# Kernel tuning notes

Hardware: AMD Instinct MI355X
Metric: run time of the kernel (lower is better)

Reference implementation:

```python
import jax, jax.numpy as jnp
import numpy as np

B, S, D = 16, 1024, 384
H, DH = 6, 64  # head_dim = hidden // heads


def setup_inputs() -> dict:
    key = jax.random.key(0)
    ks = jax.random.split(key, 9)
    std = 0.02
    return {
        "x": jax.random.normal(ks[0], (B, S, D), jnp.float32),
        "Wq": jax.random.normal(ks[1], (H, D, DH), jnp.float32) * std,
        "bq": jax.random.normal(ks[2], (H, DH), jnp.float32) * std,
        "Wk": jax.random.normal(ks[3], (H, D, DH), jnp.float32) * std,
        "bk": jax.random.normal(ks[4], (H, DH), jnp.float32) * std,
        "Wv": jax.random.normal(ks[5], (H, D, DH), jnp.float32) * std,
        "bv": jax.random.normal(ks[6], (H, DH), jnp.float32) * std,
        "Wo": jax.random.normal(ks[7], (D, D), jnp.float32) * std,  # [out, in] like nn.Linear
        "bo": jax.random.normal(ks[8], (D,), jnp.float32) * std,
    }


def reference(x, Wq, bq, Wk, bk, Wv, bv, Wo, bo):
    # Per-head q/k/v projections (stacked over heads h)
    q = jnp.einsum("bsd,hde->bhse", x, Wq) + bq[None, :, None, :]
    k = jnp.einsum("bsd,hde->bhse", x, Wk) + bk[None, :, None, :]
    v = jnp.einsum("bsd,hde->bhse", x, Wv) + bv[None, :, None, :]
    # Explicit softmax attention (dropout prob = 0.0 in config)
    scores = jnp.einsum("bhse,bhte->bhst", q, k) / jnp.sqrt(jnp.float32(DH))
    probs = jax.nn.softmax(scores, axis=-1)
    ctx = jnp.einsum("bhst,bhte->bhse", probs, v)  # [B,H,S,DH]
    # Concat heads along last dim: [B,S,H*DH]
    concat = jnp.transpose(ctx, (0, 2, 1, 3)).reshape(B, S, H * DH)
    # Output projection (nn.Linear: y = x @ W^T + b)
    out = jnp.einsum("bsd,ed->bse", concat, Wo) + bo
    return out
```

## Files before the change

kernel.cpp:

```cpp
#include <hip/hip_runtime.h>
#include <hip/hip_bf16.h>

typedef __attribute__((ext_vector_type(8))) short short8;
typedef __attribute__((ext_vector_type(4))) short short4v;
typedef __attribute__((ext_vector_type(4))) float float4v;
typedef __attribute__((ext_vector_type(4))) int int4v;

#define MFMA16(a,b,c) __builtin_amdgcn_mfma_f32_16x16x32_bf16((a),(b),(c),0,0,0)
#define EXP2(x) __builtin_amdgcn_exp2f(x)

static constexpr int Bz = 16, Sq = 1024, Dm = 384, Hh = 6, Dh = 64;
static constexpr int Mtok = Bz * Sq;
static constexpr int NQKV = 1152;

__device__ __forceinline__ short f2bf(float f) {
  union { float f; unsigned u; } v; v.f = f;
  unsigned r = v.u + 0x7fffu + ((v.u >> 16) & 1u);
  return (short)(r >> 16);
}

__device__ __forceinline__ unsigned cvtpk(float a, float b) {
  unsigned d;
  asm("v_cvt_pk_bf16_f32 %0, %1, %2" : "=v"(d) : "v"(a), "v"(b));
  return d;
}

__device__ __forceinline__ void gload16(const void* src, void* lds) {
  __builtin_amdgcn_global_load_lds(
      (const __attribute__((address_space(1))) unsigned int*)src,
      (__attribute__((address_space(3))) unsigned int*)lds, 16, 0, 0);
}

__device__ __forceinline__ int vperm(int s) {
  return (s & ~31) | ((s & 12) << 1) | ((s & 16) >> 2) | (s & 3);
}

__global__ __launch_bounds__(256) void conv_x(const float* __restrict__ x,
                                              short* __restrict__ xb) {
  const int i = (blockIdx.x * 256 + threadIdx.x) * 8;
  float4v v0 = *(const float4v*)(x + i);
  float4v v1 = *(const float4v*)(x + i + 4);
  short8 o;
  o[0] = f2bf(v0[0]); o[1] = f2bf(v0[1]); o[2] = f2bf(v0[2]); o[3] = f2bf(v0[3]);
  o[4] = f2bf(v1[0]); o[5] = f2bf(v1[1]); o[6] = f2bf(v1[2]); o[7] = f2bf(v1[3]);
  *(short8*)(xb + i) = o;
}

__global__ __launch_bounds__(256) void conv_w(const float* __restrict__ Wq,
                                              const float* __restrict__ Wk,
                                              const float* __restrict__ Wv,
                                              const float* __restrict__ bq,
                                              const float* __restrict__ bk,
                                              const float* __restrict__ bv,
                                              const float* __restrict__ Wo,
                                              short* __restrict__ Wt,
                                              float* __restrict__ bias,
                                              short* __restrict__ Wob) {
  const float SCL = 0.125f * 1.44269504088896340736f;
  const int i = blockIdx.x * 256 + threadIdx.x;
  const int NW = NQKV * Dm;
  if (i < NW) {
    const int c = i / Dm, d = i % Dm;
    const int p = c / 384, rr = c % 384;
    const int h = rr >> 6, dh = rr & 63;
    const float* W = (p == 0) ? Wq : ((p == 1) ? Wk : Wv);
    float w = W[(h * Dm + d) * Dh + dh];
    if (p == 0) w *= SCL;
    Wt[c * Dm + d] = f2bf(w);
  } else if (i < NW + NQKV) {
    const int c = i - NW;
    const int p = c / 384, rr = c % 384;
    const int h = rr >> 6, dh = rr & 63;
    const float* bb = (p == 0) ? bq : ((p == 1) ? bk : bv);
    float b = bb[h * Dh + dh];
    if (p == 0) b *= SCL;
    bias[c] = b;
  } else if (i < NW + NQKV + Dm * Dm) {
    const int j = i - NW - NQKV;
    Wob[j] = f2bf(Wo[j]);
  }
}


__global__ __launch_bounds__(256) void qkv_gemm(const short* __restrict__ Xb,
                                                const short* __restrict__ Wt,
                                                const float* __restrict__ bias,
                                                short* __restrict__ qkv,
                                                short* __restrict__ vt) {
  __shared__ char smem[49152];
  const int tid = threadIdx.x;
  const int wave = tid >> 6, lane = tid & 63;
  const int r = lane & 15, g = lane >> 4;
  const int wr = wave >> 1, wc = wave & 1;

  const int flat = blockIdx.x;
  const int w = (flat & 7) * 144 + (flat >> 3);
  const int bx = w % 9, by = w / 9;
  const int bm0 = by * 128, bn0 = bx * 128;
  const int m0 = bm0 + wr * 64, n0 = bn0 + wc * 64;

  float bv_n[4];
#pragma unroll
  for (int ni = 0; ni < 4; ++ni) bv_n[ni] = bias[n0 + ni * 16 + r];
  asm volatile("s_waitcnt vmcnt(0)" ::: "memory");

  const char *aSrc0, *aSrc1, *bSrc0, *bSrc1;
  {
    const int o0 = tid * 16, o1 = 4096 + tid * 16;
    const int lr0 = o0 >> 7, cb0 = (o0 & 127) ^ ((lr0 & 7) << 4);
    const int lr1 = o1 >> 7, cb1 = (o1 & 127) ^ ((lr1 & 7) << 4);
    const int m_0 = 2 * lr0 + (cb0 >> 6), kb0 = cb0 & 63;
    const int m_1 = 2 * lr1 + (cb1 >> 6), kb1 = cb1 & 63;
    aSrc0 = (const char*)(Xb + (bm0 + m_0) * Dm) + kb0;
    aSrc1 = (const char*)(Xb + (bm0 + m_1) * Dm) + kb1;
    bSrc0 = (const char*)(Wt + (bn0 + m_0) * Dm) + kb0;
    bSrc1 = (const char*)(Wt + (bn0 + m_1) * Dm) + kb1;
  }
  auto stage = [&](int t, int buf) {
    char* base = smem + buf * 16384;
    const int kb = t * 64;
    gload16(aSrc0 + kb, base + wave * 1024);
    gload16(aSrc1 + kb, base + 4096 + wave * 1024);
    gload16(bSrc0 + kb, base + 8192 + wave * 1024);
    gload16(bSrc1 + kb, base + 12288 + wave * 1024);
  };

  int aOff[4], bOff[4];
#pragma unroll
  for (int i = 0; i < 4; ++i) {
    const int m = wr * 64 + i * 16 + r;
    const int lr = m >> 1;
    aOff[i] = lr * 128 + ((((m & 1) << 6) | (16 * g)) ^ ((lr & 7) << 4));
    const int n = wc * 64 + i * 16 + r;
    const int lrn = n >> 1;
    bOff[i] = 8192 + lrn * 128 + ((((n & 1) << 6) | (16 * g)) ^ ((lrn & 7) << 4));
  }

  float4v acc[4][4] = {};
  auto compute = [&](int buf) {
    const char* sb = smem + buf * 16384;
    short8 a[4], b[4];
#pragma unroll
    for (int i = 0; i < 4; ++i) a[i] = *(const short8*)(sb + aOff[i]);
#pragma unroll
    for (int i = 0; i < 4; ++i) b[i] = *(const short8*)(sb + bOff[i]);
#pragma unroll
    for (int mi = 0; mi < 4; ++mi)
#pragma unroll
      for (int ni = 0; ni < 4; ++ni)
        acc[mi][ni] = MFMA16(a[mi], b[ni], acc[mi][ni]);
  };

  stage(0, 0);
  stage(1, 1);
  stage(2, 2);
#pragma unroll 1
  for (int t = 0; t < 10; ++t) {
    asm volatile("s_waitcnt vmcnt(8)" ::: "memory");
    __builtin_amdgcn_s_barrier();
    compute(t % 3);
    __builtin_amdgcn_s_barrier();
    if (t < 9) stage(t + 3, t % 3);
  }
  asm volatile("s_waitcnt vmcnt(4)" ::: "memory");
  __builtin_amdgcn_s_barrier();
  compute(1);
  asm volatile("s_waitcnt vmcnt(0)" ::: "memory");
  __builtin_amdgcn_s_barrier();
  compute(2);

#pragma unroll
  for (int ni = 0; ni < 4; ++ni) {
    const int col = n0 + ni * 16 + r;
    const int p = col / 384, rr2 = col % 384;
    const int h = rr2 >> 6, dh = rr2 & 63;
    const float bv = bv_n[ni];
#pragma unroll
    for (int mi = 0; mi < 4; ++mi) {
#pragma unroll
      for (int rp = 0; rp < 2; ++rp) {
        const unsigned u = cvtpk(acc[mi][ni][2 * rp] + bv,
                                 acc[mi][ni][2 * rp + 1] + bv);
        const short lo = (short)u, hi = (short)(u >> 16);
        const int mg = m0 + mi * 16 + 4 * g + 2 * rp;
        if (p < 2) {
          qkv[mg * NQKV + col] = lo;
          qkv[(mg + 1) * NQKV + col] = hi;
        } else {
          const int bb = mg >> 10, s = mg & 1023;
          const int sp = vperm(s);
          short* vp = vt + ((bb * Hh + h) * Dh + dh) * Sq;
          vp[sp] = lo;
          vp[sp + 1] = hi;
        }
      }
    }
  }
}

__global__ __launch_bounds__(256) void attn(const short* __restrict__ qkv,
                                            const short* __restrict__ vt,
                                            short* __restrict__ ctx) {
  __shared__ char smem[32768];
  const int tid = threadIdx.x;
  const int wave = tid >> 6, lane = tid & 63;
  const int r = lane & 15, g = lane >> 4;
  const int xr = (r & 7) << 4;
  const int flat = blockIdx.x;
  const int w = (flat & 7) * 96 + (flat >> 3);
  const int qb = w & 7, bh = w >> 3;
  const int b = bh / Hh, h = bh % Hh;
  const int tok0 = b * Sq;
  const int qw = qb * 128 + wave * 32;

  short8 qf[2][2];
#pragma unroll
  for (int f = 0; f < 2; ++f) {
    const short* qp = qkv + (tok0 + qw + 16 * f + r) * NQKV + h * Dh;
    qf[f][0] = *(const short8*)(qp + 8 * g);
    qf[f][1] = *(const short8*)(qp + 32 + 8 * g);
  }
  asm volatile("s_waitcnt vmcnt(0)" ::: "memory");

  const short* kg = qkv + tok0 * NQKV + 384 + h * Dh;
  const short* vg = vt + (b * Hh + h) * Dh * Sq;

  const int o0 = wave * 2048 + lane * 16;
  const int row0 = o0 >> 7, cb0 = (o0 & 127) ^ ((row0 & 7) << 4);
  const int o1 = o0 + 1024;
  const int row1 = o1 >> 7, cb1 = (o1 & 127) ^ ((row1 & 7) << 4);

#define STAGE(T, BUFSEL)                                                        \
  {                                                                             \
    char* kb_ = smem + (BUFSEL) * 16384;                                        \
    const int kv_ = (T) * 64;                                                   \
    gload16((const char*)(kg + (kv_ + row0) * NQKV) + cb0, kb_ + wave * 2048);  \
    gload16((const char*)(vg + row0 * Sq + kv_) + cb0, kb_ + 8192 + wave * 2048);\
    gload16((const char*)(kg + (kv_ + row1) * NQKV) + cb1, kb_ + wave * 2048 + 1024);\
    gload16((const char*)(vg + row1 * Sq + kv_) + cb1, kb_ + 8192 + wave * 2048 + 1024);\
  }

  int kOff[4][2], vOff[4][2];
#pragma unroll
  for (int kt = 0; kt < 4; ++kt)
#pragma unroll
    for (int c = 0; c < 2; ++c)
      kOff[kt][c] = (16 * kt + r) * 128 + ((64 * c + 16 * g) ^ xr);
#pragma unroll
  for (int d = 0; d < 4; ++d)
#pragma unroll
    for (int h2 = 0; h2 < 2; ++h2)
      vOff[d][h2] = (16 * d + r) * 128 + ((64 * h2 + 16 * g) ^ xr);

  float4v acc[4][2] = {};
  float lsum[2] = {0.f, 0.f};

  auto compute = [&](int bufsel) {
    const char* kb = smem + bufsel * 16384;
    const char* vb = kb + 8192;
    short8 kf[4][2];
#pragma unroll
    for (int kt = 0; kt < 4; ++kt) {
      kf[kt][0] = *(const short8*)(kb + kOff[kt][0]);
      kf[kt][1] = *(const short8*)(kb + kOff[kt][1]);
    }
    short8 vf[4][2];
#pragma unroll
    for (int d = 0; d < 4; ++d)
#pragma unroll
      for (int h2 = 0; h2 < 2; ++h2)
        vf[d][h2] = *(const short8*)(vb + vOff[d][h2]);
    float4v s[4][2];
    __builtin_amdgcn_s_setprio(1);
#pragma unroll
    for (int kt = 0; kt < 4; ++kt)
#pragma unroll
      for (int f = 0; f < 2; ++f) {
        float4v z = {};
        z = MFMA16(kf[kt][0], qf[f][0], z);
        z = MFMA16(kf[kt][1], qf[f][1], z);
        s[kt][f] = z;
      }
    __builtin_amdgcn_s_setprio(0);
    short8 pa[2][2];
#pragma unroll
    for (int f = 0; f < 2; ++f) {
      float ps = 0.f;
#pragma unroll
      for (int h2 = 0; h2 < 2; ++h2) {
        float e0[4], e1[4];
#pragma unroll
        for (int j = 0; j < 4; ++j) {
          e0[j] = EXP2(s[2 * h2][f][j]);
          e1[j] = EXP2(s[2 * h2 + 1][f][j]);
          ps += e0[j] + e1[j];
        }
        int4v wv;
        wv[0] = (int)cvtpk(e0[0], e0[1]);
        wv[1] = (int)cvtpk(e0[2], e0[3]);
        wv[2] = (int)cvtpk(e1[0], e1[1]);
        wv[3] = (int)cvtpk(e1[2], e1[3]);
        pa[f][h2] = __builtin_bit_cast(short8, wv);
      }
      lsum[f] += ps;
    }
    __builtin_amdgcn_s_setprio(1);
#pragma unroll
    for (int d = 0; d < 4; ++d)
#pragma unroll
      for (int f = 0; f < 2; ++f) {
        acc[d][f] = MFMA16(pa[f][0], vf[d][0], acc[d][f]);
        acc[d][f] = MFMA16(pa[f][1], vf[d][1], acc[d][f]);
      }
    __builtin_amdgcn_s_setprio(0);
  };

  STAGE(0, 0)
  STAGE(1, 1)
#pragma unroll 1
  for (int t = 0; t < 15; ++t) {
    asm volatile("s_waitcnt vmcnt(4)" ::: "memory");
    __builtin_amdgcn_s_barrier();
    compute(t & 1);
    __builtin_amdgcn_s_barrier();
    if (t < 14) STAGE(t + 2, t & 1)
  }
  asm volatile("s_waitcnt vmcnt(0)" ::: "memory");
  __builtin_amdgcn_s_barrier();
  compute(1);

#pragma unroll
  for (int f = 0; f < 2; ++f) {
    lsum[f] += __shfl_xor(lsum[f], 16);
    lsum[f] += __shfl_xor(lsum[f], 32);
  }
#pragma unroll
  for (int f = 0; f < 2; ++f) {
    float il[4];
#pragma unroll
    for (int reg = 0; reg < 4; ++reg) il[reg] = 1.f / __shfl(lsum[f], 4 * g + reg);
#pragma unroll
    for (int d = 0; d < 4; ++d) {
      short* cp = ctx + (tok0 + qw + 16 * f + 4 * g) * Dm + h * Dh + 16 * d + r;
#pragma unroll
      for (int reg = 0; reg < 4; ++reg)
        cp[reg * Dm] = f2bf(acc[d][f][reg] * il[reg]);
    }
  }
}

__global__ __launch_bounds__(256) void out_gemm(const short* __restrict__ ctx,
                                                const short* __restrict__ Wob,
                                                const float* __restrict__ bo,
                                                float* __restrict__ out) {
  __shared__ char smem[49152];
  const int tid = threadIdx.x;
  const int wave = tid >> 6, lane = tid & 63;
  const int r = lane & 15, g = lane >> 4;
  const int wr = wave >> 1, wc = wave & 1;

  const int flat = blockIdx.x;
  const int w = (flat & 7) * 48 + (flat >> 3);
  const int bx = w % 3, by = w / 3;
  const int bm0 = by * 128, bn0 = bx * 128;
  const int m0 = bm0 + wr * 64, n0 = bn0 + wc * 64;

  float bv_n[4];
#pragma unroll
  for (int ni = 0; ni < 4; ++ni) bv_n[ni] = bo[n0 + ni * 16 + r];
  asm volatile("s_waitcnt vmcnt(0)" ::: "memory");

  const char *aSrc0, *aSrc1, *bSrc0, *bSrc1;
  {
    const int o0 = tid * 16, o1 = 4096 + tid * 16;
    const int lr0 = o0 >> 7, cb0 = (o0 & 127) ^ ((lr0 & 7) << 4);
    const int lr1 = o1 >> 7, cb1 = (o1 & 127) ^ ((lr1 & 7) << 4);
    const int m_0 = 2 * lr0 + (cb0 >> 6), kb0 = cb0 & 63;
    const int m_1 = 2 * lr1 + (cb1 >> 6), kb1 = cb1 & 63;
    aSrc0 = (const char*)(ctx + (bm0 + m_0) * Dm) + kb0;
    aSrc1 = (const char*)(ctx + (bm0 + m_1) * Dm) + kb1;
    bSrc0 = (const char*)(Wob + (bn0 + m_0) * Dm) + kb0;
    bSrc1 = (const char*)(Wob + (bn0 + m_1) * Dm) + kb1;
  }
  auto stage = [&](int t, int buf) {
    char* base = smem + buf * 16384;
    const int kb = t * 64;
    gload16(aSrc0 + kb, base + wave * 1024);
    gload16(aSrc1 + kb, base + 4096 + wave * 1024);
    gload16(bSrc0 + kb, base + 8192 + wave * 1024);
    gload16(bSrc1 + kb, base + 12288 + wave * 1024);
  };

  int aOff[4], bOff[4];
#pragma unroll
  for (int i = 0; i < 4; ++i) {
    const int m = wr * 64 + i * 16 + r;
    const int lr = m >> 1;
    aOff[i] = lr * 128 + ((((m & 1) << 6) | (16 * g)) ^ ((lr & 7) << 4));
    const int n = wc * 64 + i * 16 + r;
    const int lrn = n >> 1;
    bOff[i] = 8192 + lrn * 128 + ((((n & 1) << 6) | (16 * g)) ^ ((lrn & 7) << 4));
  }

  float4v acc[4][4] = {};
  auto compute = [&](int buf) {
    const char* sb = smem + buf * 16384;
    short8 a[4], b[4];
#pragma unroll
    for (int i = 0; i < 4; ++i) a[i] = *(const short8*)(sb + aOff[i]);
#pragma unroll
    for (int i = 0; i < 4; ++i) b[i] = *(const short8*)(sb + bOff[i]);
#pragma unroll
    for (int mi = 0; mi < 4; ++mi)
#pragma unroll
      for (int ni = 0; ni < 4; ++ni)
        acc[mi][ni] = MFMA16(a[mi], b[ni], acc[mi][ni]);
  };

  stage(0, 0);
  stage(1, 1);
  stage(2, 2);
#pragma unroll 1
  for (int t = 0; t < 10; ++t) {
    asm volatile("s_waitcnt vmcnt(8)" ::: "memory");
    __builtin_amdgcn_s_barrier();
    compute(t % 3);
    __builtin_amdgcn_s_barrier();
    if (t < 9) stage(t + 3, t % 3);
  }
  asm volatile("s_waitcnt vmcnt(4)" ::: "memory");
  __builtin_amdgcn_s_barrier();
  compute(1);
  asm volatile("s_waitcnt vmcnt(0)" ::: "memory");
  __builtin_amdgcn_s_barrier();
  compute(2);

#pragma unroll
  for (int ni = 0; ni < 4; ++ni) {
    const int col = n0 + ni * 16 + r;
    const float bv = bv_n[ni];
#pragma unroll
    for (int mi = 0; mi < 4; ++mi) {
#pragma unroll
      for (int reg = 0; reg < 4; ++reg) {
        const int mg = m0 + mi * 16 + 4 * g + reg;
        out[mg * Dm + col] = acc[mi][ni][reg] + bv;
      }
    }
  }
}

extern "C" void kernel_launch(void* const* d_in, const int* in_sizes, int n_in,
                              void* d_out, int out_size, void* d_ws, size_t ws_size,
                              hipStream_t stream) {
  const float* x  = (const float*)d_in[0];
  const float* Wq = (const float*)d_in[1];
  const float* bq = (const float*)d_in[2];
  const float* Wk = (const float*)d_in[3];
  const float* bk = (const float*)d_in[4];
  const float* Wv = (const float*)d_in[5];
  const float* bv = (const float*)d_in[6];
  const float* Wo = (const float*)d_in[7];
  const float* bo = (const float*)d_in[8];
  float* out = (float*)d_out;

  char* ws = (char*)d_ws;
  short* Xb   = (short*)(ws);
  short* Wt   = (short*)(ws + 12582912);
  float* bias = (float*)(ws + 13467648);
  short* Wob  = (short*)(ws + 13472256);
  short* qkv  = (short*)(ws + 13767168);
  short* vt   = (short*)(ws + 51515904);
  short* ctx  = (short*)(ws + 64098816);

  conv_x<<<Mtok * Dm / (256 * 8), 256, 0, stream>>>(x, Xb);
  conv_w<<<(NQKV * Dm + NQKV + Dm * Dm + 255) / 256, 256, 0, stream>>>(
      Wq, Wk, Wv, bq, bk, bv, Wo, Wt, bias, Wob);
  qkv_gemm<<<1152, 256, 0, stream>>>(Xb, Wt, bias, qkv, vt);
  attn<<<768, 256, 0, stream>>>(qkv, vt, ctx);
  out_gemm<<<384, 256, 0, stream>>>(ctx, Wob, bo, out);
}
```

Before: 100.4 us.

## Use 3-buffer single-barrier pipelines and compute softmax row sums via MFMA

All three kernels move from a pattern of two barriers per iteration to triple buffering. Each iteration issues the load two tiles ahead into the third buffer, so only one barrier per iteration is needed. The attention kernel grows its LDS to 48KB to hold three K/V stages. It also replaces the scalar exp-sum accumulation and the cross-lane shuffle reduction with extra MFMAs against a vector of bf16 ones, which yields the row sums directly in the accumulator layout. This removes VALU adds and the shuffles but adds MFMA work, and the row sums are now taken from bf16-rounded probabilities.

```diff
diff --git a/kernel.cpp b/kernel.cpp
--- a/kernel.cpp
+++ b/kernel.cpp
@@ -153,14 +153,12 @@
 
   stage(0, 0);
   stage(1, 1);
-  stage(2, 2);
 #pragma unroll 1
   for (int t = 0; t < 10; ++t) {
-    asm volatile("s_waitcnt vmcnt(8)" ::: "memory");
+    asm volatile("s_waitcnt vmcnt(4)" ::: "memory");
     __builtin_amdgcn_s_barrier();
     compute(t % 3);
-    __builtin_amdgcn_s_barrier();
-    if (t < 9) stage(t + 3, t % 3);
+    stage(t + 2, (t + 2) % 3);
   }
   asm volatile("s_waitcnt vmcnt(4)" ::: "memory");
   __builtin_amdgcn_s_barrier();
@@ -201,7 +199,7 @@
 __global__ __launch_bounds__(256) void attn(const short* __restrict__ qkv,
                                             const short* __restrict__ vt,
                                             short* __restrict__ ctx) {
-  __shared__ char smem[32768];
+  __shared__ char smem[49152];
   const int tid = threadIdx.x;
   const int wave = tid >> 6, lane = tid & 63;
   const int r = lane & 15, g = lane >> 4;
@@ -252,8 +250,12 @@
     for (int h2 = 0; h2 < 2; ++h2)
       vOff[d][h2] = (16 * d + r) * 128 + ((64 * h2 + 16 * g) ^ xr);
 
+  short8 ones;
+#pragma unroll
+  for (int j = 0; j < 8; ++j) ones[j] = (short)0x3F80;
+
   float4v acc[4][2] = {};
-  float lsum[2] = {0.f, 0.f};
+  float4v lacc[2] = {};
 
   auto compute = [&](int bufsel) {
     const char* kb = smem + bufsel * 16384;
@@ -284,26 +286,16 @@
     __builtin_amdgcn_s_setprio(0);
     short8 pa[2][2];
 #pragma unroll
-    for (int f = 0; f < 2; ++f) {
-      float ps = 0.f;
+    for (int f = 0; f < 2; ++f)
 #pragma unroll
       for (int h2 = 0; h2 < 2; ++h2) {
-        float e0[4], e1[4];
-#pragma unroll
-        for (int j = 0; j < 4; ++j) {
-          e0[j] = EXP2(s[2 * h2][f][j]);
-          e1[j] = EXP2(s[2 * h2 + 1][f][j]);
-          ps += e0[j] + e1[j];
-        }
         int4v wv;
-        wv[0] = (int)cvtpk(e0[0], e0[1]);
-        wv[1] = (int)cvtpk(e0[2], e0[3]);
-        wv[2] = (int)cvtpk(e1[0], e1[1]);
-        wv[3] = (int)cvtpk(e1[2], e1[3]);
+        wv[0] = (int)cvtpk(EXP2(s[2 * h2][f][0]), EXP2(s[2 * h2][f][1]));
+        wv[1] = (int)cvtpk(EXP2(s[2 * h2][f][2]), EXP2(s[2 * h2][f][3]));
+        wv[2] = (int)cvtpk(EXP2(s[2 * h2 + 1][f][0]), EXP2(s[2 * h2 + 1][f][1]));
+        wv[3] = (int)cvtpk(EXP2(s[2 * h2 + 1][f][2]), EXP2(s[2 * h2 + 1][f][3]));
         pa[f][h2] = __builtin_bit_cast(short8, wv);
       }
-      lsum[f] += ps;
-    }
     __builtin_amdgcn_s_setprio(1);
 #pragma unroll
     for (int d = 0; d < 4; ++d)
@@ -312,33 +304,35 @@
         acc[d][f] = MFMA16(pa[f][0], vf[d][0], acc[d][f]);
         acc[d][f] = MFMA16(pa[f][1], vf[d][1], acc[d][f]);
       }
+#pragma unroll
+    for (int f = 0; f < 2; ++f) {
+      lacc[f] = MFMA16(pa[f][0], ones, lacc[f]);
+      lacc[f] = MFMA16(pa[f][1], ones, lacc[f]);
+    }
     __builtin_amdgcn_s_setprio(0);
   };
 
   STAGE(0, 0)
   STAGE(1, 1)
 #pragma unroll 1
-  for (int t = 0; t < 15; ++t) {
+  for (int t = 0; t < 14; ++t) {
     asm volatile("s_waitcnt vmcnt(4)" ::: "memory");
     __builtin_amdgcn_s_barrier();
-    compute(t & 1);
-    __builtin_amdgcn_s_barrier();
-    if (t < 14) STAGE(t + 2, t & 1)
-  }
-  asm volatile("s_waitcnt vmcnt(0)" ::: "memory");
-  __builtin_amdgcn_s_barrier();
-  compute(1);
-
-#pragma unroll
-  for (int f = 0; f < 2; ++f) {
-    lsum[f] += __shfl_xor(lsum[f], 16);
-    lsum[f] += __shfl_xor(lsum[f], 32);
-  }
+    compute(t % 3);
+    STAGE(t + 2, (t + 2) % 3)
+  }
+  asm volatile("s_waitcnt vmcnt(4)" ::: "memory");
+  __builtin_amdgcn_s_barrier();
+  compute(2);
+  asm volatile("s_waitcnt vmcnt(0)" ::: "memory");
+  __builtin_amdgcn_s_barrier();
+  compute(0);
+
 #pragma unroll
   for (int f = 0; f < 2; ++f) {
     float il[4];
 #pragma unroll
-    for (int reg = 0; reg < 4; ++reg) il[reg] = 1.f / __shfl(lsum[f], 4 * g + reg);
+    for (int reg = 0; reg < 4; ++reg) il[reg] = 1.f / lacc[f][reg];
 #pragma unroll
     for (int d = 0; d < 4; ++d) {
       short* cp = ctx + (tok0 + qw + 16 * f + 4 * g) * Dm + h * Dh + 16 * d + r;
@@ -419,14 +413,12 @@
 
   stage(0, 0);
   stage(1, 1);
-  stage(2, 2);
 #pragma unroll 1
   for (int t = 0; t < 10; ++t) {
-    asm volatile("s_waitcnt vmcnt(8)" ::: "memory");
+    asm volatile("s_waitcnt vmcnt(4)" ::: "memory");
     __builtin_amdgcn_s_barrier();
     compute(t % 3);
-    __builtin_amdgcn_s_barrier();
-    if (t < 9) stage(t + 3, t % 3);
+    stage(t + 2, (t + 2) % 3);
   }
   asm volatile("s_waitcnt vmcnt(4)" ::: "memory");
   __builtin_amdgcn_s_barrier();
```

New measurement: 97.02 us. 1.03x faster.
